# Kernel optimization log

Hardware: AMD Instinct MI355X
Metric: run time of the kernel (lower is better)

The kernel has to match this reference:

```python
import jax, jax.numpy as jnp
from jax import lax
import numpy as np

B, C_IN, H, W = 8, 1024, 64, 64
DI, C_OUT = 512, 1024
BN_EPS = 1e-5


def setup_inputs() -> dict:
    key = jax.random.key(0)
    ks = jax.random.split(key, 5)
    std = 0.01  # torch init.normal_(std=0.01)
    return {
        "x": jax.random.normal(ks[0], (B, C_IN, H, W), jnp.float32),
        "theta_w": jax.random.normal(ks[1], (DI, C_IN), jnp.float32) * std,
        "theta_b": jnp.zeros((DI,), jnp.float32),
        "phi_w": jax.random.normal(ks[2], (DI, C_IN), jnp.float32) * std,
        "phi_b": jnp.zeros((DI,), jnp.float32),
        "g_w": jax.random.normal(ks[3], (DI, C_IN), jnp.float32) * std,
        "g_b": jnp.zeros((DI,), jnp.float32),
        "out_w": jax.random.normal(ks[4], (C_OUT, DI), jnp.float32) * std,
        "out_b": jnp.zeros((C_OUT,), jnp.float32),
        "bn_w": jnp.ones((C_OUT,), jnp.float32),
        "bn_b": jnp.zeros((C_OUT,), jnp.float32),
    }


def _conv1x1(x, w, b):
    # x: [b,c,h,w], w: [o,c] -> [b,o,h,w]
    return jnp.einsum('bchw,oc->bohw', x, w) + b[None, :, None, None]


def reference(x, theta_w, theta_b, phi_w, phi_b, g_w, g_b, out_w, out_b, bn_w, bn_b):
    b, c, h, w = x.shape
    di = theta_w.shape[0]

    theta = _conv1x1(x, theta_w, theta_b).reshape(b, di, h * w)  # [b,di,N]

    # MaxPool2d(kernel=2, stride=2)
    pool = lax.reduce_window(x, -jnp.inf, lax.max,
                             (1, 1, 2, 2), (1, 1, 2, 2), 'VALID')
    phi = _conv1x1(pool, phi_w, phi_b).reshape(b, di, -1)   # [b,di,M]
    g = _conv1x1(pool, g_w, g_b).reshape(b, di, -1)          # [b,di,M]

    # scaled dot-product attention: scores [b,N,M]
    scores = jnp.einsum('bdn,bdm->bnm', theta, phi) * (di ** -0.5)
    p = jax.nn.softmax(scores, axis=-1)

    # t_x = g @ p^T  -> [b,di,N]
    t = jnp.einsum('bdm,bnm->bdn', g, p).reshape(b, di, h, w)

    y = _conv1x1(t, out_w, out_b)  # [b,C_out,h,w]

    # BatchNorm2d (training mode: batch statistics, biased variance)
    mean = jnp.mean(y, axis=(0, 2, 3), keepdims=True)
    var = jnp.var(y, axis=(0, 2, 3), keepdims=True)
    y = (y - mean) * lax.rsqrt(var + BN_EPS)
    y = y * bn_w[None, :, None, None] + bn_b[None, :, None, None]

    return y + x
```

## Files before the change

kernel.cpp:

```cpp
#include <hip/hip_runtime.h>
#include <cstdint>

typedef unsigned short u16;
typedef __attribute__((ext_vector_type(4))) unsigned short u16x4;
typedef __attribute__((ext_vector_type(8))) short short8;
typedef __attribute__((ext_vector_type(4))) float f32x4;

#define DI 512
#define CIN 1024
#define NPIX 4096
#define MPIX 1024

__device__ __forceinline__ float bf2f(u16 u) {
  union { unsigned int i; float f; } v; v.i = ((unsigned int)u) << 16; return v.f;
}
__device__ __forceinline__ u16 f2bf(float f) {
  union { float f; unsigned int i; } v; v.f = f;
  unsigned int r = v.i + 0x7fffu + ((v.i >> 16) & 1u);
  return (u16)(r >> 16);
}
__device__ __forceinline__ void unpack8(uint4 v, float* f) {
  union { unsigned int i; float f; } u;
  u.i = v.x << 16;          f[0] = u.f;
  u.i = v.x & 0xffff0000u;  f[1] = u.f;
  u.i = v.y << 16;          f[2] = u.f;
  u.i = v.y & 0xffff0000u;  f[3] = u.f;
  u.i = v.z << 16;          f[4] = u.f;
  u.i = v.z & 0xffff0000u;  f[5] = u.f;
  u.i = v.w << 16;          f[6] = u.f;
  u.i = v.w & 0xffff0000u;  f[7] = u.f;
}

__device__ __forceinline__ void gload16(const u16* g, u16* l) {
  __builtin_amdgcn_global_load_lds(
      (const __attribute__((address_space(1))) void*)g,
      (__attribute__((address_space(3))) void*)l, 16, 0, 0);
}

__global__ __launch_bounds__(256) void cvt4_kernel(
    const float* __restrict__ s0, const float* __restrict__ s1,
    const float* __restrict__ s2, const float* __restrict__ s3,
    u16* __restrict__ d0, u16* __restrict__ d1,
    u16* __restrict__ d2, u16* __restrict__ d3) {
  int i = blockIdx.x * 256 + threadIdx.x;
  int sel = i >> 17;
  int j = i & 131071;
  const float* src = sel == 0 ? s0 : sel == 1 ? s1 : sel == 2 ? s2 : s3;
  u16* dst = sel == 0 ? d0 : sel == 1 ? d1 : sel == 2 ? d2 : d3;
  float4 v = *(const float4*)(src + (long)j * 4);
  u16x4 w;
  w[0] = f2bf(v.x); w[1] = f2bf(v.y); w[2] = f2bf(v.z); w[3] = f2bf(v.w);
  *(u16x4*)(dst + (long)j * 4) = w;
}

__global__ __launch_bounds__(256) void transpose_pool_kernel(
    const float* __restrict__ x, u16* __restrict__ xT, u16* __restrict__ poolT) {
  __shared__ u16 tile[64][136];
  const int b = blockIdx.z;
  const int n0 = blockIdx.x * 128, c0 = blockIdx.y * 64;
  const float* xb = x + (long)b * CIN * NPIX;
  u16* xTb = xT + (long)b * NPIX * CIN;
  const int t = threadIdx.x;
  const int tc = t >> 5, tn = (t & 31) * 4;
  #pragma unroll
  for (int i = 0; i < 8; i++) {
    int c = tc + i * 8;
    float4 v = *(const float4*)(xb + (long)(c0 + c) * NPIX + n0 + tn);
    tile[c][tn + 0] = f2bf(v.x);
    tile[c][tn + 1] = f2bf(v.y);
    tile[c][tn + 2] = f2bf(v.z);
    tile[c][tn + 3] = f2bf(v.w);
  }
  __syncthreads();
  const int tn2 = t >> 4, tc2 = (t & 15) * 4;
  #pragma unroll
  for (int i = 0; i < 8; i++) {
    int n = tn2 + i * 16;
    u16x4 w;
    w[0] = tile[tc2 + 0][n];
    w[1] = tile[tc2 + 1][n];
    w[2] = tile[tc2 + 2][n];
    w[3] = tile[tc2 + 3][n];
    *(u16x4*)(xTb + (long)(n0 + n) * CIN + c0 + tc2) = w;
  }
  const int j = t >> 3, c8 = (t & 7) * 8;
  u16 r[8] __attribute__((aligned(16)));
  #pragma unroll
  for (int k = 0; k < 8; k++) {
    int c = c8 + k;
    float m0 = fmaxf(bf2f(tile[c][2 * j]), bf2f(tile[c][2 * j + 1]));
    float m1 = fmaxf(bf2f(tile[c][64 + 2 * j]), bf2f(tile[c][64 + 2 * j + 1]));
    r[k] = f2bf(fmaxf(m0, m1));
  }
  *(uint4*)(poolT + ((long)b * MPIX + blockIdx.x * 32 + j) * CIN + c0 + c8) =
      *(uint4*)r;
}

template<int OM, bool HAS_BIAS, bool HAS_CS, bool HAS_SHIFT, bool HAS_EXP, bool HAS_PSUM2>
__global__ __launch_bounds__(256)
void gemm_tn(const u16* __restrict__ A, const u16* __restrict__ B,
             void* __restrict__ Cv,
             const float* __restrict__ bias, long sBias,
             const float* __restrict__ cs, long sCS,
             const float* __restrict__ shift, long sShift,
             float* __restrict__ psum_out,
             float scale, int M, int N, int K, long sA, long sB, long sC)
{
  A += blockIdx.z * sA;
  B += blockIdx.z * sB;
  if (HAS_BIAS) bias += blockIdx.z * sBias;
  if (HAS_CS) cs += blockIdx.z * sCS;
  if (HAS_SHIFT) shift += blockIdx.z * sShift;
  const int bm = blockIdx.y * 128;
  const int bn = blockIdx.x * 128;
  __shared__ __align__(16) u16 As[128 * 64];
  __shared__ __align__(16) u16 Bs[128 * 64];
  __shared__ float psum[4][128];
  const int tid = threadIdx.x;
  const int lane = tid & 63;
  const int wave = tid >> 6;
  const int wm = (wave >> 1) * 64;
  const int wn = (wave & 1) * 64;
  const int lr = lane & 15;
  const int q  = lane >> 4;
  const int sxor = lane & 7;
  f32x4 acc[4][4] = {};

  const int swz = ((lane & 7) ^ (lane >> 3)) * 8;
  const long grow = 32 * wave + (lane >> 3);
  const u16* Ag = A + ((long)bm + grow) * K + swz;
  const u16* Bg = B + ((long)bn + grow) * K + swz;

  for (int kt = 0; kt < K; kt += 64) {
    __syncthreads();
    #pragma unroll
    for (int i = 0; i < 4; i++) {
      gload16(Ag + (long)(8 * i) * K + kt, &As[(wave * 4 + i) * 512]);
      gload16(Bg + (long)(8 * i) * K + kt, &Bs[(wave * 4 + i) * 512]);
    }
    __syncthreads();
    #pragma unroll
    for (int kk = 0; kk < 2; kk++) {
      short8 av[4], bv[4];
      #pragma unroll
      for (int mi = 0; mi < 4; mi++)
        av[mi] = *(const short8*)&As[(wm + mi * 16 + lr) * 64 +
                                     (((kk << 2) + q) ^ sxor) * 8];
      #pragma unroll
      for (int ni = 0; ni < 4; ni++)
        bv[ni] = *(const short8*)&Bs[(wn + ni * 16 + lr) * 64 +
                                     (((kk << 2) + q) ^ sxor) * 8];
      #pragma unroll
      for (int mi = 0; mi < 4; mi++) {
        #pragma unroll
        for (int ni = 0; ni < 4; ni++)
          acc[mi][ni] = __builtin_amdgcn_mfma_f32_16x16x32_bf16(
              av[mi], bv[ni], acc[mi][ni], 0, 0, 0);
      }
    }
  }

  const int dr = (lane >> 4) * 4;
  float rowsum[4][4];
  float rowsq[4][4];
  if (HAS_EXP || HAS_PSUM2) {
    #pragma unroll
    for (int mi = 0; mi < 4; mi++)
      #pragma unroll
      for (int r = 0; r < 4; r++) { rowsum[mi][r] = 0.f; rowsq[mi][r] = 0.f; }
  }
  #pragma unroll
  for (int mi = 0; mi < 4; mi++) {
    const int rowb = bm + wm + mi * 16 + dr;
    float bvs[4] = {0.f, 0.f, 0.f, 0.f};
    float shv[4] = {0.f, 0.f, 0.f, 0.f};
    if (HAS_BIAS) {
      #pragma unroll
      for (int r = 0; r < 4; r++) bvs[r] = bias[rowb + r];
    }
    if (HAS_SHIFT) {
      #pragma unroll
      for (int r = 0; r < 4; r++) shv[r] = shift[rowb + r];
    }
    #pragma unroll
    for (int ni = 0; ni < 4; ni++) {
      const int col = bn + wn + ni * 16 + lr;
      const float csv = HAS_CS ? cs[col] : 1.0f;
      float v[4];
      #pragma unroll
      for (int r = 0; r < 4; r++) {
        float t = acc[mi][ni][r] * scale;
        if (HAS_CS) t *= csv;
        if (HAS_SHIFT) t -= shv[r];
        if (HAS_BIAS) t += bvs[r];
        if (HAS_EXP) t = expf(t);
        if (HAS_EXP || HAS_PSUM2) rowsum[mi][r] += t;
        if (HAS_PSUM2) rowsq[mi][r] += t * t;
        v[r] = t;
      }
      if (OM == 1) {
        u16* C = (u16*)Cv + blockIdx.z * sC;
        u16x4 w;
        #pragma unroll
        for (int r = 0; r < 4; r++) w[r] = f2bf(v[r]);
        *(u16x4*)(C + (long)col * M + rowb) = w;
      } else if (OM == 0) {
        u16* C = (u16*)Cv + blockIdx.z * sC;
        #pragma unroll
        for (int r = 0; r < 4; r++)
          C[(long)(rowb + r) * N + col] = f2bf(v[r]);
      } else {
        float* C = (float*)Cv + blockIdx.z * sC;
        #pragma unroll
        for (int r = 0; r < 4; r++)
          C[(long)(rowb + r) * N + col] = v[r];
      }
    }
  }
  if (HAS_EXP || HAS_PSUM2) {
    #pragma unroll
    for (int msk = 1; msk < 16; msk <<= 1)
      #pragma unroll
      for (int mi = 0; mi < 4; mi++)
        #pragma unroll
        for (int r = 0; r < 4; r++) {
          rowsum[mi][r] += __shfl_xor(rowsum[mi][r], msk);
          if (HAS_PSUM2) rowsq[mi][r] += __shfl_xor(rowsq[mi][r], msk);
        }
    if ((lane & 15) == 0) {
      #pragma unroll
      for (int mi = 0; mi < 4; mi++)
        #pragma unroll
        for (int r = 0; r < 4; r++) {
          psum[wave & 1][wm + mi * 16 + dr + r] = rowsum[mi][r];
          if (HAS_PSUM2) psum[2 + (wave & 1)][wm + mi * 16 + dr + r] = rowsq[mi][r];
        }
    }
    __syncthreads();
    if (tid < 128) {
      if (HAS_EXP)
        psum_out[((long)blockIdx.z * gridDim.x + blockIdx.x) * 4096 + bm + tid] =
            psum[0][tid] + psum[1][tid];
      if (HAS_PSUM2) {
        const long blk = ((long)blockIdx.z * gridDim.y + blockIdx.y) * gridDim.x
                         + blockIdx.x;
        psum_out[blk * 256 + tid] = psum[0][tid] + psum[1][tid];
        psum_out[blk * 256 + 128 + tid] = psum[2][tid] + psum[3][tid];
      }
    }
  }
}

__global__ __launch_bounds__(256) void inv_kernel(const float* __restrict__ partial,
                                                  float* __restrict__ inv) {
  const int idx = blockIdx.x * 256 + threadIdx.x;
  const int b = idx >> 12, n = idx & 4095;
  const float* p = partial + (long)b * 32768 + n;
  float s = 0.f;
  #pragma unroll
  for (int x = 0; x < 8; x++) s += p[(long)x * 4096];
  inv[idx] = 1.0f / s;
}

__global__ __launch_bounds__(256) void gbar_kernel(const u16* __restrict__ g_n,
                                                   float* __restrict__ gbar) {
  const int row = blockIdx.x * 4 + (threadIdx.x >> 6);
  const int lane = threadIdx.x & 63;
  const long base = (long)row * MPIX + lane * 16;
  uint4 va = *(const uint4*)(g_n + base);
  uint4 vb = *(const uint4*)(g_n + base + 8);
  float f[16];
  unpack8(va, f); unpack8(vb, f + 8);
  float s = 0.f;
  #pragma unroll
  for (int j = 0; j < 16; j++) s += f[j];
  #pragma unroll
  for (int off = 32; off > 0; off >>= 1) s += __shfl_xor(s, off);
  if (lane == 0) gbar[row] = s * (1.0f / 1024.0f);
}

__global__ __launch_bounds__(256) void c0_kernel(const float* __restrict__ out_w,
                                                 const float* __restrict__ out_b,
                                                 const float* __restrict__ gbar,
                                                 float* __restrict__ c0) {
  const int idx = blockIdx.x * 4 + (threadIdx.x >> 6);
  const int lane = threadIdx.x & 63;
  const int b = idx >> 10, c = idx & 1023;
  const int d0 = lane * 8;
  float4 w0 = *(const float4*)(out_w + (long)c * DI + d0);
  float4 w1 = *(const float4*)(out_w + (long)c * DI + d0 + 4);
  float4 g0 = *(const float4*)(gbar + (long)b * DI + d0);
  float4 g1 = *(const float4*)(gbar + (long)b * DI + d0 + 4);
  float s = w0.x * g0.x + w0.y * g0.y + w0.z * g0.z + w0.w * g0.w
          + w1.x * g1.x + w1.y * g1.y + w1.z * g1.z + w1.w * g1.w;
  #pragma unroll
  for (int off = 32; off > 0; off >>= 1) s += __shfl_xor(s, off);
  if (lane == 0) c0[idx] = out_b[c] + s;
}

__global__ __launch_bounds__(256) void stats2_kernel(const float* __restrict__ partial,
                                                     const float* __restrict__ c0,
                                                     float* __restrict__ stats) {
  const int co = blockIdx.x * 256 + threadIdx.x;
  const int by = co >> 7, r = co & 127;
  float sd = 0.f, sd2 = 0.f, sbc = 0.f;
  for (int b = 0; b < 8; b++) {
    float sb = 0.f, qb = 0.f;
    #pragma unroll
    for (int bx = 0; bx < 32; bx++) {
      const long blk = (((long)b * 8 + by) * 32 + bx) * 256;
      sb += partial[blk + r];
      qb += partial[blk + 128 + r];
    }
    sd += sb; sd2 += qb;
    sbc += c0[b * 1024 + co] * sb;
  }
  float sc0 = 0.f, sc02 = 0.f;
  #pragma unroll
  for (int b = 0; b < 8; b++) {
    float c = c0[b * 1024 + co];
    sc0 += c; sc02 += c * c;
  }
  stats[co] = 4096.0f * sc0 + sd;
  stats[1024 + co] = 4096.0f * sc02 + 2.0f * sbc + sd2;
}

__global__ __launch_bounds__(256) void final_kernel(const u16* __restrict__ dy,
    const float* __restrict__ x, const float* __restrict__ stats,
    const float* __restrict__ c0,
    const float* __restrict__ bnw, const float* __restrict__ bnb,
    float* __restrict__ out) {
  const int bc = blockIdx.x;
  const int co = bc & 1023;
  const float mean = stats[co] * (1.0f / 32768.0f);
  const float var = stats[1024 + co] * (1.0f / 32768.0f) - mean * mean;
  const float inv = rsqrtf(var + 1e-5f) * bnw[co];
  const float addc = bnb[co] - mean * inv + c0[bc] * inv;
  const long base = (long)bc * 4096;
  const int t = threadIdx.x;
  #pragma unroll
  for (int i = 0; i < 2; i++) {
    const long off = base + (long)(i * 256 + t) * 8;
    uint4 v = *(const uint4*)(dy + off);
    float f[8]; unpack8(v, f);
    const float4 x0 = *(const float4*)(x + off);
    const float4 x1 = *(const float4*)(x + off + 4);
    float4 o0, o1;
    o0.x = f[0] * inv + addc + x0.x;
    o0.y = f[1] * inv + addc + x0.y;
    o0.z = f[2] * inv + addc + x0.z;
    o0.w = f[3] * inv + addc + x0.w;
    o1.x = f[4] * inv + addc + x1.x;
    o1.y = f[5] * inv + addc + x1.y;
    o1.z = f[6] * inv + addc + x1.z;
    o1.w = f[7] * inv + addc + x1.w;
    *(float4*)(out + off) = o0;
    *(float4*)(out + off + 4) = o1;
  }
}

extern "C" void kernel_launch(void* const* d_in, const int* in_sizes, int n_in,
                              void* d_out, int out_size, void* d_ws, size_t ws_size,
                              hipStream_t stream) {
  (void)in_sizes; (void)n_in; (void)out_size; (void)ws_size;
  const float* x       = (const float*)d_in[0];
  const float* theta_w = (const float*)d_in[1];
  const float* theta_b = (const float*)d_in[2];
  const float* phi_w   = (const float*)d_in[3];
  const float* phi_b   = (const float*)d_in[4];
  const float* g_w     = (const float*)d_in[5];
  const float* g_b     = (const float*)d_in[6];
  const float* out_w   = (const float*)d_in[7];
  const float* out_b   = (const float*)d_in[8];
  const float* bn_w    = (const float*)d_in[9];
  const float* bn_b    = (const float*)d_in[10];
  float* out = (float*)d_out;
  char* ws = (char*)d_ws;
  const size_t MB = 1024 * 1024;

  u16* xT     = (u16*)(ws + 0 * MB);
  u16* poolT  = (u16*)(ws + 64 * MB);
  u16* w_th   = (u16*)(ws + 80 * MB);
  u16* w_ph   = (u16*)(ws + 81 * MB);
  u16* w_g    = (u16*)(ws + 82 * MB);
  u16* thetaT = (u16*)(ws + 84 * MB);
  u16* phiT   = (u16*)(ws + 116 * MB);
  u16* g_n    = (u16*)(ws + 124 * MB);
  u16* e      = (u16*)(ws + 132 * MB);
  u16* tT     = (u16*)(ws + 196 * MB);
  u16* w_out  = (u16*)(ws + 228 * MB);
  float* inv_s = (float*)(ws + 229 * MB);
  float* gbar  = (float*)(ws + 229 * MB + 131072);
  float* c0b   = (float*)(ws + 229 * MB + 147456);
  float* stats = (float*)(ws + 229 * MB + 180224);
  float* partial = (float*)(ws + 230 * MB);
  float* partial2 = (float*)(ws + 231 * MB);
  u16* dy = xT;

  cvt4_kernel<<<2048, 256, 0, stream>>>(theta_w, phi_w, g_w, out_w,
                                        w_th, w_ph, w_g, w_out);
  transpose_pool_kernel<<<dim3(32, 16, 8), 256, 0, stream>>>(x, xT, poolT);
  gemm_tn<1, true, false, false, false, false><<<dim3(32, 4, 8), 256, 0, stream>>>(
      w_th, xT, thetaT, theta_b, 0L, nullptr, 0L, nullptr, 0L, nullptr,
      1.0f, 512, 4096, 1024, 0L, (long)NPIX * CIN, (long)NPIX * DI);
  gemm_tn<1, true, false, false, false, false><<<dim3(8, 4, 8), 256, 0, stream>>>(
      w_ph, poolT, phiT, phi_b, 0L, nullptr, 0L, nullptr, 0L, nullptr,
      1.0f, 512, 1024, 1024, 0L, (long)MPIX * CIN, (long)MPIX * DI);
  gemm_tn<0, true, false, false, false, false><<<dim3(8, 4, 8), 256, 0, stream>>>(
      w_g, poolT, g_n, g_b, 0L, nullptr, 0L, nullptr, 0L, nullptr,
      1.0f, 512, 1024, 1024, 0L, (long)MPIX * CIN, (long)DI * MPIX);
  gbar_kernel<<<1024, 256, 0, stream>>>(g_n, gbar);
  c0_kernel<<<2048, 256, 0, stream>>>(out_w, out_b, gbar, c0b);
  gemm_tn<0, false, false, false, true, false><<<dim3(8, 32, 8), 256, 0, stream>>>(
      thetaT, phiT, e, nullptr, 0L, nullptr, 0L, nullptr, 0L, partial,
      0.044194173824159216f, 4096, 1024, 512,
      (long)NPIX * DI, (long)MPIX * DI, (long)NPIX * MPIX);
  inv_kernel<<<128, 256, 0, stream>>>(partial, inv_s);
  gemm_tn<1, false, true, true, false, false><<<dim3(32, 4, 8), 256, 0, stream>>>(
      g_n, e, tT, nullptr, 0L, inv_s, 4096L, gbar, 512L, nullptr,
      1.0f, 512, 4096, 1024,
      (long)DI * MPIX, (long)NPIX * MPIX, (long)NPIX * DI);
  gemm_tn<0, false, false, false, false, true><<<dim3(32, 8, 8), 256, 0, stream>>>(
      w_out, tT, dy, nullptr, 0L, nullptr, 0L, nullptr, 0L, partial2,
      1.0f, 1024, 4096, 512, 0L, (long)NPIX * DI, (long)1024 * NPIX);
  stats2_kernel<<<4, 256, 0, stream>>>(partial2, c0b, stats);
  final_kernel<<<8192, 256, 0, stream>>>(dy, x, stats, c0b, bn_w, bn_b, out);
}
```

Baseline: 387.4 us.

## Stage GEMM epilogue through shared memory for coalesced stores; split transpose and pool

The GEMM epilogue now writes each 128x128 output tile into shared memory, reusing the A/B staging buffers, with an XOR swizzle for the transposed layout. It then stores the tile to global memory as coalesced 16-byte vectors instead of scattered 2-byte or 8-byte stores. The target is the large bf16 outputs such as the attention matrix, where strided narrow stores waste memory bandwidth. The fused transpose+maxpool kernel is also split into a smaller-tile transpose and a separate pool kernel that reads the transposed bf16 data. That split adds an extra pass over the activation and one more launch, and the float (OM==2) output path is removed, so every output is now written as bf16.

```diff
diff --git a/kernel.cpp b/kernel.cpp
--- a/kernel.cpp
+++ b/kernel.cpp
@@ -53,18 +53,18 @@
   *(u16x4*)(dst + (long)j * 4) = w;
 }
 
-__global__ __launch_bounds__(256) void transpose_pool_kernel(
-    const float* __restrict__ x, u16* __restrict__ xT, u16* __restrict__ poolT) {
-  __shared__ u16 tile[64][136];
+__global__ __launch_bounds__(256) void transpose_kernel(const float* __restrict__ x,
+                                                        u16* __restrict__ xT) {
+  __shared__ u16 tile[64][72];
   const int b = blockIdx.z;
-  const int n0 = blockIdx.x * 128, c0 = blockIdx.y * 64;
+  const int n0 = blockIdx.x * 64, c0 = blockIdx.y * 64;
   const float* xb = x + (long)b * CIN * NPIX;
   u16* xTb = xT + (long)b * NPIX * CIN;
   const int t = threadIdx.x;
-  const int tc = t >> 5, tn = (t & 31) * 4;
-  #pragma unroll
-  for (int i = 0; i < 8; i++) {
-    int c = tc + i * 8;
+  const int tc = t >> 4, tn = (t & 15) * 4;
+  #pragma unroll
+  for (int i = 0; i < 4; i++) {
+    int c = tc + i * 16;
     float4 v = *(const float4*)(xb + (long)(c0 + c) * NPIX + n0 + tn);
     tile[c][tn + 0] = f2bf(v.x);
     tile[c][tn + 1] = f2bf(v.y);
@@ -74,7 +74,7 @@
   __syncthreads();
   const int tn2 = t >> 4, tc2 = (t & 15) * 4;
   #pragma unroll
-  for (int i = 0; i < 8; i++) {
+  for (int i = 0; i < 4; i++) {
     int n = tn2 + i * 16;
     u16x4 w;
     w[0] = tile[tc2 + 0][n];
@@ -83,17 +83,30 @@
     w[3] = tile[tc2 + 3][n];
     *(u16x4*)(xTb + (long)(n0 + n) * CIN + c0 + tc2) = w;
   }
-  const int j = t >> 3, c8 = (t & 7) * 8;
+}
+
+__global__ __launch_bounds__(256) void pool_kernel(const u16* __restrict__ xT,
+                                                   u16* __restrict__ poolT) {
+  const int idx = blockIdx.x * 256 + threadIdx.x;
+  const int cc = (idx & 127) * 8;
+  const int m = (idx >> 7) & 1023;
+  const int b = idx >> 17;
+  const int i = m >> 5, j = m & 31;
+  const int n1 = (i * 2) * 64 + j * 2;
+  const u16* base = xT + (long)b * NPIX * CIN + cc;
+  uint4 v0 = *(const uint4*)(base + (long)(n1) * CIN);
+  uint4 v1 = *(const uint4*)(base + (long)(n1 + 1) * CIN);
+  uint4 v2 = *(const uint4*)(base + (long)(n1 + 64) * CIN);
+  uint4 v3 = *(const uint4*)(base + (long)(n1 + 65) * CIN);
+  float f0[8], f1[8], f2[8], f3[8];
+  unpack8(v0, f0); unpack8(v1, f1); unpack8(v2, f2); unpack8(v3, f3);
   u16 r[8] __attribute__((aligned(16)));
   #pragma unroll
   for (int k = 0; k < 8; k++) {
-    int c = c8 + k;
-    float m0 = fmaxf(bf2f(tile[c][2 * j]), bf2f(tile[c][2 * j + 1]));
-    float m1 = fmaxf(bf2f(tile[c][64 + 2 * j]), bf2f(tile[c][64 + 2 * j + 1]));
-    r[k] = f2bf(fmaxf(m0, m1));
-  }
-  *(uint4*)(poolT + ((long)b * MPIX + blockIdx.x * 32 + j) * CIN + c0 + c8) =
-      *(uint4*)r;
+    float mx = fmaxf(fmaxf(f0[k], f1[k]), fmaxf(f2[k], f3[k]));
+    r[k] = f2bf(mx);
+  }
+  *(uint4*)(poolT + ((long)b * MPIX + m) * CIN + cc) = *(uint4*)r;
 }
 
 template<int OM, bool HAS_BIAS, bool HAS_CS, bool HAS_SHIFT, bool HAS_EXP, bool HAS_PSUM2>
@@ -113,8 +126,9 @@
   if (HAS_SHIFT) shift += blockIdx.z * sShift;
   const int bm = blockIdx.y * 128;
   const int bn = blockIdx.x * 128;
-  __shared__ __align__(16) u16 As[128 * 64];
-  __shared__ __align__(16) u16 Bs[128 * 64];
+  __shared__ __align__(16) u16 smem[128 * 128];
+  u16* As = smem;
+  u16* Bs = smem + 128 * 64;
   __shared__ float psum[4][128];
   const int tid = threadIdx.x;
   const int lane = tid & 63;
@@ -160,6 +174,7 @@
     }
   }
 
+  __syncthreads();
   const int dr = (lane >> 4) * 4;
   float rowsum[4][4];
   float rowsq[4][4];
@@ -171,7 +186,8 @@
   }
   #pragma unroll
   for (int mi = 0; mi < 4; mi++) {
-    const int rowb = bm + wm + mi * 16 + dr;
+    const int rowl = wm + mi * 16 + dr;
+    const int rowb = bm + rowl;
     float bvs[4] = {0.f, 0.f, 0.f, 0.f};
     float shv[4] = {0.f, 0.f, 0.f, 0.f};
     if (HAS_BIAS) {
@@ -184,8 +200,8 @@
     }
     #pragma unroll
     for (int ni = 0; ni < 4; ni++) {
-      const int col = bn + wn + ni * 16 + lr;
-      const float csv = HAS_CS ? cs[col] : 1.0f;
+      const int coll = wn + ni * 16 + lr;
+      const float csv = HAS_CS ? cs[bn + coll] : 1.0f;
       float v[4];
       #pragma unroll
       for (int r = 0; r < 4; r++) {
@@ -199,21 +215,14 @@
         v[r] = t;
       }
       if (OM == 1) {
-        u16* C = (u16*)Cv + blockIdx.z * sC;
         u16x4 w;
         #pragma unroll
         for (int r = 0; r < 4; r++) w[r] = f2bf(v[r]);
-        *(u16x4*)(C + (long)col * M + rowb) = w;
-      } else if (OM == 0) {
-        u16* C = (u16*)Cv + blockIdx.z * sC;
+        unsigned bo = (unsigned)((coll * 128 + rowl) * 2) ^ ((coll & 7) << 4);
+        *(u16x4*)((char*)smem + bo) = w;
+      } else {
         #pragma unroll
-        for (int r = 0; r < 4; r++)
-          C[(long)(rowb + r) * N + col] = f2bf(v[r]);
-      } else {
-        float* C = (float*)Cv + blockIdx.z * sC;
-        #pragma unroll
-        for (int r = 0; r < 4; r++)
-          C[(long)(rowb + r) * N + col] = v[r];
+        for (int r = 0; r < 4; r++) smem[(rowl + r) * 128 + coll] = f2bf(v[r]);
       }
     }
   }
@@ -236,7 +245,28 @@
           if (HAS_PSUM2) psum[2 + (wave & 1)][wm + mi * 16 + dr + r] = rowsq[mi][r];
         }
     }
-    __syncthreads();
+  }
+  __syncthreads();
+  u16* C = (u16*)Cv + blockIdx.z * sC;
+  if (OM == 1) {
+    #pragma unroll
+    for (int i = 0; i < 8; i++) {
+      const int chunk = i * 256 + tid;
+      const int coll = chunk >> 4, rq = chunk & 15;
+      unsigned bo = (unsigned)(coll * 256 + rq * 16) ^ ((coll & 7) << 4);
+      uint4 w = *(const uint4*)((const char*)smem + bo);
+      *(uint4*)(C + (long)(bn + coll) * M + bm + rq * 8) = w;
+    }
+  } else {
+    #pragma unroll
+    for (int i = 0; i < 8; i++) {
+      const int chunk = i * 256 + tid;
+      const int row = chunk >> 4, cq = chunk & 15;
+      uint4 w = *(const uint4*)(smem + row * 128 + cq * 8);
+      *(uint4*)(C + (long)(bm + row) * N + bn + cq * 8) = w;
+    }
+  }
+  if (HAS_EXP || HAS_PSUM2) {
     if (tid < 128) {
       if (HAS_EXP)
         psum_out[((long)blockIdx.z * gridDim.x + blockIdx.x) * 4096 + bm + tid] =
@@ -399,7 +429,8 @@
 
   cvt4_kernel<<<2048, 256, 0, stream>>>(theta_w, phi_w, g_w, out_w,
                                         w_th, w_ph, w_g, w_out);
-  transpose_pool_kernel<<<dim3(32, 16, 8), 256, 0, stream>>>(x, xT, poolT);
+  transpose_kernel<<<dim3(64, 16, 8), 256, 0, stream>>>(x, xT);
+  pool_kernel<<<4096, 256, 0, stream>>>(xT, poolT);
   gemm_tn<1, true, false, false, false, false><<<dim3(32, 4, 8), 256, 0, stream>>>(
       w_th, xT, thetaT, theta_b, 0L, nullptr, 0L, nullptr, 0L, nullptr,
       1.0f, 512, 4096, 1024, 0L, (long)NPIX * CIN, (long)NPIX * DI);
```

New measurement: 384.3 us. About the same (-0.8%).
